# Kernel optimization log

Measured on AMD Instinct MI355X. Metric: run time of the kernel, lower is better.

## Reference

```python
import jax, jax.numpy as jnp
import numpy as np

B = 256
IN_CH = 1
E = 8          # embedding_channels (power of 2)
DEPTH = 3      # log2(E)
T = 8192       # time_range
WINDOW = 2.0
K = 15         # kernel_size (odd -> torch 'same' == lax 'SAME')
TPI = 2.0 * np.pi


def conv1d(x, w, b, dilation=1, groups=1):
    # x: (B, Cin, T), w: (Cout, Cin/groups, K), b: (Cout,)
    out = jax.lax.conv_general_dilated(
        x, w, window_strides=(1,), padding='SAME',
        rhs_dilation=(dilation,),
        dimension_numbers=('NCH', 'OIH', 'NCH'),
        feature_group_count=groups)
    return out + b[None, :, None]


def setup_inputs() -> dict:
    key = jax.random.key(0)
    ks = jax.random.split(key, 14)
    s = 0.05
    x = jax.random.normal(ks[0], (B, T), jnp.float32)
    W1 = jax.random.normal(ks[1], (E, 2, 1, K), jnp.float32) * s   # per-channel Conv1d(1,2)
    b1 = jax.random.normal(ks[2], (E, 2), jnp.float32) * s
    W2 = jax.random.normal(ks[3], (E, 1, 2, K), jnp.float32) * s   # per-channel Conv1d(2,1)
    b2 = jax.random.normal(ks[4], (E, 1), jnp.float32) * s
    fcW = jax.random.normal(ks[5], (E, 2, T), jnp.float32) * 0.01  # per-channel Linear(T, 2)
    fcb = jax.random.normal(ks[6], (E, 2), jnp.float32) * s
    # deconv tree: level j has 2**(DEPTH-1-j) Conv1d(2,1) units, stacked as grouped conv
    dW0 = jax.random.normal(ks[7], (4, 2, K), jnp.float32) * s
    db0 = jax.random.normal(ks[8], (4,), jnp.float32) * s
    dW1 = jax.random.normal(ks[9], (2, 2, K), jnp.float32) * s
    db1 = jax.random.normal(ks[10], (2,), jnp.float32) * s
    dW2 = jax.random.normal(ks[11], (1, 2, K), jnp.float32) * s
    db2 = jax.random.normal(ks[12], (1,), jnp.float32) * s
    return dict(x=x, W1=W1, b1=b1, W2=W2, b2=b2, fcW=fcW, fcb=fcb,
                dW0=dW0, db0=db0, dW1=dW1, db1=db1, dW2=dW2, db2=db2)


def reference(x, W1, b1, W2, b2, fcW, fcb, dW0, db0, dW1, db1, dW2, db2):
    y = x.reshape(x.shape[0], IN_CH, T)
    # per-channel dilated conv stack (dilation = 2**i)
    chans = []
    for i in range(E):
        h = conv1d(y, W1[i], b1[i], dilation=2 ** i)
        chans.append(conv1d(h, W2[i], b2[i], dilation=2 ** i))
    latent = jnp.concatenate(chans, axis=1)                # (B, E, T)
    # FFT -> frequency / amplitude / offset
    rfft = jnp.fft.rfft(latent, axis=2)                    # (B, E, T//2+1)
    power = jnp.abs(rfft[:, :, 1:]) ** 2
    freqs = jnp.asarray(np.fft.rfftfreq(T)[1:] * T / WINDOW, jnp.float32)
    psum = jnp.sum(power, axis=2)
    f = jnp.sum(freqs * power, axis=2) / psum              # (B, E)
    a = 2.0 * jnp.sqrt(psum) / T
    b_off = rfft.real[:, :, 0] / T
    # per-channel Linear(T, 2) -> phase
    v = jnp.einsum('bet,ect->bec', latent, fcW) + fcb      # (B, E, 2)
    p = jnp.arctan2(v[..., 1], v[..., 0]) / TPI            # (B, E)
    # sinusoid reconstruction
    args = jnp.linspace(-WINDOW / 2, WINDOW / 2, T, dtype=jnp.float32)
    sig = a[..., None] * jnp.sin(TPI * (f[..., None] * args + p[..., None])) + b_off[..., None]
    # deconv tree: pairs of channels -> grouped conv, halving channels each level
    y = sig
    for dW, db in ((dW0, db0), (dW1, db1), (dW2, db2)):
        y = conv1d(y, dW, db, dilation=1, groups=dW.shape[0])
    out = y.reshape(y.shape[0], IN_CH * T)
    return (out, latent, sig,
            p[..., None], f[..., None], a[..., None], b_off[..., None])
```

## Files before the change

kernel.cpp:

```cpp
#include <hip/hip_runtime.h>
#include <math.h>

#define TT 8192
#define BB 256
#define EE 8
#define KK 15
#define PI_F  3.14159265358979323846f
#define TPI_F 6.28318530717958647692f

#define OFF_OUT 0
#define OFF_LAT (BB*TT)
#define OFF_SIG (OFF_LAT + BB*EE*TT)
#define OFF_P   (OFF_SIG + BB*EE*TT)
#define OFF_F   (OFF_P + BB*EE)
#define OFF_A   (OFF_F + BB*EE)
#define OFF_B0  (OFF_A + BB*EE)

#define TILE_C 1024

#define SWZ(i) ((i) + ((i) >> 5))

__global__ __launch_bounds__(512) void conv_stack_kernel(
    const float* __restrict__ x, const float* __restrict__ W1,
    const float* __restrict__ b1, const float* __restrict__ W2,
    const float* __restrict__ b2, float* __restrict__ latent)
{
  extern __shared__ float smem[];
  const int e = blockIdx.x, b = blockIdx.y;
  const int d  = 1 << e;
  const int M  = TT >> e;
  const int Lp = (M <= 64) ? 92 : ((((M + 47) >> 5) << 5) + 12);
  float* sxp = smem;
  float* hbF = smem + d * Lp;
  float* hbL = hbF + 14 * d;
  float* sW  = hbL + 14 * d;
  const int tid = threadIdx.x;
  const float* xr = x + b * TT;

  const int nstage = TT + 28 * d;
  for (int i = tid; i < nstage; i += 512) {
    int t  = i - 14 * d;
    int ph = i & (d - 1);
    int n  = i >> e;
    sxp[ph * Lp + n] = (t >= 0 && t < TT) ? xr[t] : 0.0f;
  }

  if (tid < 29) {
    float acc = 0.0f;
    for (int c = 0; c < 2; c++) {
      const float* w1 = W1 + e*30 + c*15;
      const float* w2 = W2 + e*30 + c*15;
      int jlo = tid - 14; if (jlo < 0) jlo = 0;
      int jhi = tid;      if (jhi > 14) jhi = 14;
      for (int j = jlo; j <= jhi; j++) acc += w2[j] * w1[tid - j];
    }
    sW[tid] = acc;
  } else if (tid == 29) {
    float s20 = 0.f, s21 = 0.f;
    for (int j = 0; j < 15; j++) { s20 += W2[e*30 + j]; s21 += W2[e*30 + 15 + j]; }
    sW[29] = b2[e] + s20*b1[e*2] + s21*b1[e*2 + 1];
  } else if (tid >= 32 && tid < 62) {
    sW[tid] = W1[e*30 + (tid - 32)];
  } else if (tid >= 64 && tid < 94) {
    sW[tid] = W2[e*30 + (tid - 64)];
  } else if (tid == 94 || tid == 95) {
    sW[tid] = b1[e*2 + (tid - 94)];
  }
  __syncthreads();

  for (int idx = tid; idx < 28 * d; idx += 512) {
    int q = idx;
    int lastf = (q >= 14 * d);
    if (lastf) q -= 14 * d;
    int c  = (q >= 7 * d) ? 1 : 0;
    int u  = c ? (q - 7 * d) : q;
    int ph = u & (d - 1);
    int nbase = lastf ? (M + 7) : 0;
    const float* bp = &sxp[ph * Lp + (u >> e) + nbase];
    float h = sW[94 + c];
    #pragma unroll
    for (int k = 0; k < 15; k++) h = fmaf(sW[32 + c*15 + k], bp[k], h);
    (lastf ? hbL : hbF)[c * 7 * d + u] = h;
  }

  float W[29];
  #pragma unroll
  for (int s = 0; s < 29; s++) W[s] = sW[s];
  const float Bc = sW[29];
  __syncthreads();

  float* lr = latent + (b * EE + e) * TT;
  #pragma unroll 1
  for (int g = 0; g < 4; g++) {
    const int vt = g * 512 + tid;
    const int ph = vt & (d - 1);
    const int m0 = (vt >> e) << 2;

    float win[32];
    {
      const float4* wp = (const float4*)&sxp[ph * Lp + m0];
      #pragma unroll
      for (int v = 0; v < 8; v++) {
        float4 qv = wp[v];
        win[4*v] = qv.x; win[4*v+1] = qv.y; win[4*v+2] = qv.z; win[4*v+3] = qv.w;
      }
    }
    float acc[4] = {Bc, Bc, Bc, Bc};
    #pragma unroll
    for (int s = 0; s < 29; s++) {
      #pragma unroll
      for (int r = 0; r < 4; r++) acc[r] = fmaf(W[s], win[s + r], acc[r]);
    }

    if (m0 <= 6) {
      #pragma unroll
      for (int r = 0; r < 4; r++) {
        int m = m0 + r;
        if (m <= 6) {
          float corr = 0.0f;
          for (int j = 0; j <= 6 - m; j++) {
            int ih = ph + (m + j) * d;
            corr = fmaf(sW[64 + j], hbF[ih], corr);
            corr = fmaf(sW[79 + j], hbF[7*d + ih], corr);
          }
          acc[r] -= corr;
        }
      }
    }
    if (m0 + 3 >= M - 7) {
      #pragma unroll
      for (int r = 0; r < 4; r++) {
        int m = m0 + r;
        if (m >= M - 7) {
          float corr = 0.0f;
          for (int j = M + 7 - m; j < 15; j++) {
            int ih = ph + (m + j - 7 - M) * d;
            corr = fmaf(sW[64 + j], hbL[ih], corr);
            corr = fmaf(sW[79 + j], hbL[7*d + ih], corr);
          }
          acc[r] -= corr;
        }
      }
    }

    #pragma unroll
    for (int r = 0; r < 4; r++) lr[ph + (m0 + r) * d] = acc[r];
  }
}

#define NF 4096

__device__ __forceinline__ int rev4(int k) {
  unsigned r = __brev((unsigned)k) >> 20;
  return (int)(((r & 0x555u) << 1) | ((r >> 1) & 0x555u));
}

__global__ __launch_bounds__(512) void fft_kernel(
    const float* __restrict__ latent, const float* __restrict__ fcW,
    const float* __restrict__ fcb, float* __restrict__ outP,
    float* __restrict__ outF, float* __restrict__ outA, float* __restrict__ outB0)
{
  __shared__ float re[SWZ(NF - 1) + 1];
  __shared__ float im[SWZ(NF - 1) + 1];
  __shared__ float rbuf[32];
  const int e = blockIdx.x, b = blockIdx.y, tid = threadIdx.x;
  const float2* row2 = (const float2*)(latent + (b*EE + e)*TT);
  const float2* f02  = (const float2*)(fcW + (e*2 + 0)*TT);
  const float2* f12  = (const float2*)(fcW + (e*2 + 1)*TT);

  float v0 = 0.f, v1 = 0.f;
  for (int n = tid; n < NF; n += 512) {
    float2 z = row2[n];
    re[SWZ(n)] = z.x; im[SWZ(n)] = z.y;
    float2 a0 = f02[n], a1 = f12[n];
    v0 = fmaf(z.x, a0.x, v0); v0 = fmaf(z.y, a0.y, v0);
    v1 = fmaf(z.x, a1.x, v1); v1 = fmaf(z.y, a1.y, v1);
  }
  __syncthreads();

  for (int L = NF >> 2; L >= 1; L >>= 2) {
    float wstep = -1.57079632679f / (float)L;
    for (int u = tid; u < (NF >> 2); u += 512) {
      int p = u & (L - 1);
      int base = ((u - p) << 2) + p;
      int i0 = SWZ(base), i1 = SWZ(base + L), i2 = SWZ(base + 2*L), i3 = SWZ(base + 3*L);
      float ar = re[i0], ai = im[i0];
      float br = re[i1], bi = im[i1];
      float cr = re[i2], ci = im[i2];
      float dr = re[i3], di = im[i3];
      float t0r = ar + cr, t0i = ai + ci;
      float t1r = ar - cr, t1i = ai - ci;
      float t2r = br + dr, t2i = bi + di;
      float t3r = br - dr, t3i = bi - di;
      float A0r = t0r + t2r, A0i = t0i + t2i;
      float A1r = t1r + t3i, A1i = t1i - t3r;
      float A2r = t0r - t2r, A2i = t0i - t2i;
      float A3r = t1r - t3i, A3i = t1i + t3r;
      float ang = wstep * (float)p;
      float s1 = __sinf(ang), c1 = __cosf(ang);
      float c2 = c1*c1 - s1*s1, s2 = 2.f*c1*s1;
      float c3 = c1*c2 - s1*s2, s3 = c1*s2 + s1*c2;
      re[i0] = A0r;                 im[i0] = A0i;
      re[i1] = A1r*c1 - A1i*s1;     im[i1] = A1r*s1 + A1i*c1;
      re[i2] = A2r*c2 - A2i*s2;     im[i2] = A2r*s2 + A2i*c2;
      re[i3] = A3r*c3 - A3i*s3;     im[i3] = A3r*s3 + A3i*c3;
    }
    __syncthreads();
  }

  float pacc = 0.f, facc = 0.f;
  for (int k = 1 + tid; k < NF; k += 512) {
    int jk = SWZ(rev4(k));
    int jm = SWZ(rev4(NF - k));
    float zr = re[jk], zi = im[jk];
    float yr = re[jm], yi = im[jm];
    float Er = 0.5f*(zr + yr), Ei = 0.5f*(zi - yi);
    float Dr = 0.5f*(zr - yr), Di = 0.5f*(zi + yi);
    float Or = Di, Oi = -Dr;
    float ang = -PI_F * (float)k / (float)NF;
    float s = __sinf(ang), c = __cosf(ang);
    float Xr = Er + c*Or - s*Oi;
    float Xi = Ei + c*Oi + s*Or;
    float mag = fmaf(Xr, Xr, Xi*Xi);
    pacc += mag;
    facc = fmaf(0.5f * (float)k, mag, facc);
  }
  if (tid == 0) {
    float X = re[SWZ(0)] - im[SWZ(0)];
    pacc += X*X;
    facc += 2048.0f * X*X;
  }

  #pragma unroll
  for (int off = 32; off > 0; off >>= 1) {
    pacc += __shfl_down(pacc, off);
    facc += __shfl_down(facc, off);
    v0   += __shfl_down(v0, off);
    v1   += __shfl_down(v1, off);
  }
  int wid = tid >> 6, lane = tid & 63;
  if (lane == 0) {
    rbuf[wid*4 + 0] = pacc; rbuf[wid*4 + 1] = facc;
    rbuf[wid*4 + 2] = v0;   rbuf[wid*4 + 3] = v1;
  }
  __syncthreads();
  if (tid == 0) {
    float P = 0.f, Fw = 0.f, V0 = 0.f, V1 = 0.f;
    #pragma unroll
    for (int w = 0; w < 8; w++) {
      P += rbuf[w*4]; Fw += rbuf[w*4+1]; V0 += rbuf[w*4+2]; V1 += rbuf[w*4+3];
    }
    float z0r = re[SWZ(0)], z0i = im[SWZ(0)];
    float amp  = 2.0f * sqrtf(P) / (float)TT;
    float boff = (z0r + z0i) / (float)TT;
    float vv0 = V0 + fcb[e*2 + 0];
    float vv1 = V1 + fcb[e*2 + 1];
    float ph  = atan2f(vv1, vv0) / TPI_F;
    int idx = b*EE + e;
    outP[idx]  = ph;
    outF[idx]  = Fw / P;
    outA[idx]  = amp;
    outB0[idx] = boff;
  }
}

#define SST 1068
#define SL0 1056
#define SL1 1040

__global__ __launch_bounds__(256) void sig_deconv_kernel(
    const float* __restrict__ Pv, const float* __restrict__ Fv,
    const float* __restrict__ Av, const float* __restrict__ B0v,
    const float* __restrict__ dW0, const float* __restrict__ db0,
    const float* __restrict__ dW1, const float* __restrict__ db1,
    const float* __restrict__ dW2, const float* __restrict__ db2,
    float* __restrict__ sig, float* __restrict__ out)
{
  __shared__ float smem[4*SL0 + 8*SST];
  float* sl0  = smem;
  float* ssig = smem + 4*SL0;
  float* sl1  = smem + 4*SL0;

  const int tile = blockIdx.x, b = blockIdx.y;
  const int t0 = tile * TILE_C;
  const int tid = threadIdx.x;
  const float step = 2.0f / 8191.0f;

  float fs[8], am[8], psh[8], bo[8];
  #pragma unroll
  for (int ch = 0; ch < EE; ch++) {
    int idx = b*EE + ch;
    fs[ch] = Fv[idx]; am[ch] = Av[idx]; psh[ch] = Pv[idx]; bo[ch] = B0v[idx];
  }

  for (int i = tid; i < SST; i += 256) {
    int t = t0 + i - 21;
    bool in = (i < 1066 && t >= 0 && t < TT);
    float arg = fmaf(step, (float)t, -1.0f);
    bool wr = (i >= 21 && i < 21 + TILE_C);
    #pragma unroll
    for (int ch = 0; ch < EE; ch++) {
      float rr = fmaf(fs[ch], arg, psh[ch]);
      rr -= rintf(rr);
      float val = in ? fmaf(am[ch], __sinf(TPI_F * rr), bo[ch]) : 0.0f;
      ssig[ch*SST + i] = val;
      if (wr) sig[(b*EE + ch)*TT + t] = val;
    }
  }
  __syncthreads();

  for (int g = 0; g < 4; g++) {
    float bg = db0[g];
    for (int u = tid; u < 263; u += 256) {
      const float4* p0 = (const float4*)(ssig + (2*g)*SST + 4*u);
      const float4* p1 = (const float4*)(ssig + (2*g+1)*SST + 4*u);
      float w0[20], w1[20];
      #pragma unroll
      for (int v = 0; v < 5; v++) {
        float4 q0 = p0[v], q1 = p1[v];
        w0[4*v]=q0.x; w0[4*v+1]=q0.y; w0[4*v+2]=q0.z; w0[4*v+3]=q0.w;
        w1[4*v]=q1.x; w1[4*v+1]=q1.y; w1[4*v+2]=q1.z; w1[4*v+3]=q1.w;
      }
      #pragma unroll
      for (int r = 0; r < 4; r++) {
        int i0 = 4*u + r;
        int t = t0 + i0 - 14;
        float a2 = bg;
        #pragma unroll
        for (int k = 0; k < KK; k++) {
          a2 = fmaf(dW0[g*30 + k],      w0[r + k], a2);
          a2 = fmaf(dW0[g*30 + 15 + k], w1[r + k], a2);
        }
        sl0[g*SL0 + i0] = (t >= 0 && t < TT) ? a2 : 0.0f;
      }
    }
  }
  if (tid < 16) sl0[(tid >> 2)*SL0 + 1052 + (tid & 3)] = 0.0f;
  __syncthreads();

  for (int g = 0; g < 2; g++) {
    float bg = db1[g];
    for (int u = tid; u < 260; u += 256) {
      const float4* p0 = (const float4*)(sl0 + (2*g)*SL0 + 4*u);
      const float4* p1 = (const float4*)(sl0 + (2*g+1)*SL0 + 4*u);
      float w0[20], w1[20];
      #pragma unroll
      for (int v = 0; v < 5; v++) {
        float4 q0 = p0[v], q1 = p1[v];
        w0[4*v]=q0.x; w0[4*v+1]=q0.y; w0[4*v+2]=q0.z; w0[4*v+3]=q0.w;
        w1[4*v]=q1.x; w1[4*v+1]=q1.y; w1[4*v+2]=q1.z; w1[4*v+3]=q1.w;
      }
      #pragma unroll
      for (int r = 0; r < 4; r++) {
        int i1 = 4*u + r;
        if (i1 < 1038) {
          int t = t0 + i1 - 7;
          float a2 = bg;
          #pragma unroll
          for (int k = 0; k < KK; k++) {
            a2 = fmaf(dW1[g*30 + k],      w0[r + k], a2);
            a2 = fmaf(dW1[g*30 + 15 + k], w1[r + k], a2);
          }
          sl1[g*SL1 + i1] = (t >= 0 && t < TT) ? a2 : 0.0f;
        }
      }
    }
  }
  __syncthreads();

  {
    float bg = db2[0];
    float* orow = out + b*TT + t0;
    int u = tid;
    const float4* p0 = (const float4*)(sl1 + 4*u);
    const float4* p1 = (const float4*)(sl1 + SL1 + 4*u);
    float w0[20], w1[20];
    #pragma unroll
    for (int v = 0; v < 5; v++) {
      float4 q0 = p0[v], q1 = p1[v];
      w0[4*v]=q0.x; w0[4*v+1]=q0.y; w0[4*v+2]=q0.z; w0[4*v+3]=q0.w;
      w1[4*v]=q1.x; w1[4*v+1]=q1.y; w1[4*v+2]=q1.z; w1[4*v+3]=q1.w;
    }
    float4 res;
    float* resf = (float*)&res;
    #pragma unroll
    for (int r = 0; r < 4; r++) {
      float a2 = bg;
      #pragma unroll
      for (int k = 0; k < KK; k++) {
        a2 = fmaf(dW2[k],      w0[r + k], a2);
        a2 = fmaf(dW2[15 + k], w1[r + k], a2);
      }
      resf[r] = a2;
    }
    ((float4*)orow)[u] = res;
  }
}

extern "C" void kernel_launch(void* const* d_in, const int* in_sizes, int n_in,
                              void* d_out, int out_size, void* d_ws, size_t ws_size,
                              hipStream_t stream) {
  const float* x   = (const float*)d_in[0];
  const float* W1  = (const float*)d_in[1];
  const float* b1  = (const float*)d_in[2];
  const float* W2  = (const float*)d_in[3];
  const float* b2  = (const float*)d_in[4];
  const float* fcW = (const float*)d_in[5];
  const float* fcb = (const float*)d_in[6];
  const float* dW0 = (const float*)d_in[7];
  const float* db0 = (const float*)d_in[8];
  const float* dW1 = (const float*)d_in[9];
  const float* db1 = (const float*)d_in[10];
  const float* dW2 = (const float*)d_in[11];
  const float* db2 = (const float*)d_in[12];

  float* o        = (float*)d_out;
  float* out_main = o + OFF_OUT;
  float* latent   = o + OFF_LAT;
  float* sig      = o + OFF_SIG;
  float* pP  = o + OFF_P;
  float* pF  = o + OFF_F;
  float* pA  = o + OFF_A;
  float* pB0 = o + OFF_B0;

  const size_t lds_conv = 15456 * sizeof(float);
  conv_stack_kernel<<<dim3(EE, BB), 512, lds_conv, stream>>>(x, W1, b1, W2, b2, latent);
  fft_kernel<<<dim3(EE, BB), 512, 0, stream>>>(latent, fcW, fcb, pP, pF, pA, pB0);
  sig_deconv_kernel<<<dim3(TT/TILE_C, BB), 256, 0, stream>>>(
      pP, pF, pA, pB0, dW0, db0, dW1, db1, dW2, db2, sig, out_main);
}
```

Before: 347.1 us.

## Drop boundary hidden-buffer precompute, recompute edge corrections inline, shrink LDS

```diff
diff --git a/kernel.cpp b/kernel.cpp
--- a/kernel.cpp
+++ b/kernel.cpp
@@ -20,7 +20,7 @@
 
 #define SWZ(i) ((i) + ((i) >> 5))
 
-__global__ __launch_bounds__(512) void conv_stack_kernel(
+__global__ __launch_bounds__(512, 6) void conv_stack_kernel(
     const float* __restrict__ x, const float* __restrict__ W1,
     const float* __restrict__ b1, const float* __restrict__ W2,
     const float* __restrict__ b2, float* __restrict__ latent)
@@ -29,11 +29,9 @@
   const int e = blockIdx.x, b = blockIdx.y;
   const int d  = 1 << e;
   const int M  = TT >> e;
-  const int Lp = (M <= 64) ? 92 : ((((M + 47) >> 5) << 5) + 12);
+  const int Lp = ((((M - 2) + 31) >> 5) << 5) + 30;
   float* sxp = smem;
-  float* hbF = smem + d * Lp;
-  float* hbL = hbF + 14 * d;
-  float* sW  = hbL + 14 * d;
+  float* sW  = smem + d * Lp;
   const int tid = threadIdx.x;
   const float* xr = x + b * TT;
 
@@ -68,26 +66,10 @@
   }
   __syncthreads();
 
-  for (int idx = tid; idx < 28 * d; idx += 512) {
-    int q = idx;
-    int lastf = (q >= 14 * d);
-    if (lastf) q -= 14 * d;
-    int c  = (q >= 7 * d) ? 1 : 0;
-    int u  = c ? (q - 7 * d) : q;
-    int ph = u & (d - 1);
-    int nbase = lastf ? (M + 7) : 0;
-    const float* bp = &sxp[ph * Lp + (u >> e) + nbase];
-    float h = sW[94 + c];
-    #pragma unroll
-    for (int k = 0; k < 15; k++) h = fmaf(sW[32 + c*15 + k], bp[k], h);
-    (lastf ? hbL : hbF)[c * 7 * d + u] = h;
-  }
-
   float W[29];
   #pragma unroll
   for (int s = 0; s < 29; s++) W[s] = sW[s];
   const float Bc = sW[29];
-  __syncthreads();
 
   float* lr = latent + (b * EE + e) * TT;
   #pragma unroll 1
@@ -95,14 +77,15 @@
     const int vt = g * 512 + tid;
     const int ph = vt & (d - 1);
     const int m0 = (vt >> e) << 2;
+    const int row = ph * Lp;
 
     float win[32];
     {
-      const float4* wp = (const float4*)&sxp[ph * Lp + m0];
-      #pragma unroll
-      for (int v = 0; v < 8; v++) {
-        float4 qv = wp[v];
-        win[4*v] = qv.x; win[4*v+1] = qv.y; win[4*v+2] = qv.z; win[4*v+3] = qv.w;
+      const float2* wp = (const float2*)&sxp[row + m0];
+      #pragma unroll
+      for (int v = 0; v < 16; v++) {
+        float2 qv = wp[v];
+        win[2*v] = qv.x; win[2*v+1] = qv.y;
       }
     }
     float acc[4] = {Bc, Bc, Bc, Bc};
@@ -112,31 +95,50 @@
       for (int r = 0; r < 4; r++) acc[r] = fmaf(W[s], win[s + r], acc[r]);
     }
 
-    if (m0 <= 6) {
+    if (g == 0 && m0 <= 6) {
       #pragma unroll
       for (int r = 0; r < 4; r++) {
         int m = m0 + r;
         if (m <= 6) {
           float corr = 0.0f;
-          for (int j = 0; j <= 6 - m; j++) {
-            int ih = ph + (m + j) * d;
-            corr = fmaf(sW[64 + j], hbF[ih], corr);
-            corr = fmaf(sW[79 + j], hbF[7*d + ih], corr);
+          #pragma unroll
+          for (int j = 0; j < 7; j++) {
+            if (j <= 6 - m) {
+              float h0 = sW[94], h1 = sW[95];
+              #pragma unroll
+              for (int k = 0; k < 15; k++) {
+                float xv = win[r + j + k];
+                h0 = fmaf(sW[32 + k], xv, h0);
+                h1 = fmaf(sW[47 + k], xv, h1);
+              }
+              corr = fmaf(sW[64 + j], h0, corr);
+              corr = fmaf(sW[79 + j], h1, corr);
+            }
           }
           acc[r] -= corr;
         }
       }
     }
-    if (m0 + 3 >= M - 7) {
+    if (g == 3 && m0 + 3 >= M - 7) {
       #pragma unroll
       for (int r = 0; r < 4; r++) {
         int m = m0 + r;
         if (m >= M - 7) {
           float corr = 0.0f;
-          for (int j = M + 7 - m; j < 15; j++) {
-            int ih = ph + (m + j - 7 - M) * d;
-            corr = fmaf(sW[64 + j], hbL[ih], corr);
-            corr = fmaf(sW[79 + j], hbL[7*d + ih], corr);
+          #pragma unroll
+          for (int jj = 0; jj < 7; jj++) {
+            const int j = 8 + jj;
+            if (m + j >= M + 7) {
+              float h0 = sW[94], h1 = sW[95];
+              #pragma unroll
+              for (int k = 0; k < 15; k++) {
+                float xv = win[r + j + k];
+                h0 = fmaf(sW[32 + k], xv, h0);
+                h1 = fmaf(sW[47 + k], xv, h1);
+              }
+              corr = fmaf(sW[64 + j], h0, corr);
+              corr = fmaf(sW[79 + j], h1, corr);
+            }
           }
           acc[r] -= corr;
         }
@@ -423,7 +425,7 @@
   float* pA  = o + OFF_A;
   float* pB0 = o + OFF_B0;
 
-  const size_t lds_conv = 15456 * sizeof(float);
+  const size_t lds_conv = 12128 * sizeof(float);
   conv_stack_kernel<<<dim3(EE, BB), 512, lds_conv, stream>>>(x, W1, b1, W2, b2, latent);
   fft_kernel<<<dim3(EE, BB), 512, 0, stream>>>(latent, fcW, fcb, pP, pF, pA, pB0);
   sig_deconv_kernel<<<dim3(TT/TILE_C, BB), 256, 0, stream>>>(
```

Result: slower. 597.4 us (+72.1%).
